# Kernel tuning notes

Hardware: AMD Instinct MI355X
Metric: run time of the kernel (lower is better)

The kernel has to match this reference:

```python
import jax, jax.numpy as jnp
import numpy as np


def setup_inputs() -> dict:
    key = jax.random.key(0)
    ks = jax.random.split(key, 7)
    B, I, H = 16384, 1024, 1024
    s = 1.0 / np.sqrt(H)
    return {
        "x": jax.random.normal(ks[0], (B, I), jnp.float32),
        "h_prev": jax.random.normal(ks[1], (B, H), jnp.float32),
        "c_prev": jax.random.normal(ks[2], (B, H), jnp.float32),
        "Wx": jax.random.normal(ks[3], (4, H, I), jnp.float32) * s,  # gates z,i,f,o
        "bx": jax.random.normal(ks[4], (4, H), jnp.float32) * s,
        "Rh": jax.random.normal(ks[5], (4, H, H), jnp.float32) * s,
        "bh": jax.random.normal(ks[6], (4, H), jnp.float32) * s,
    }


def reference(x, h_prev, c_prev, Wx, bx, Rh, bh):
    # Fused: 2 batched GEMMs for all 4 gates, then one elementwise block.
    # gates_x[g] = x @ Wx[g].T + bx[g]  (g in z,i,f,o), same for Rh/h_prev.
    gx = jnp.einsum('bi,ghi->gbh', x, Wx) + bx[:, None, :]       # [4,B,H]
    gh = jnp.einsum('bh,gkh->gbk', h_prev, Rh) + bh[:, None, :]  # [4,B,H]
    pre = gx + gh
    z = jnp.tanh(pre[0])
    i = jax.nn.sigmoid(pre[1])
    f = jax.nn.sigmoid(pre[2])
    o = jax.nn.sigmoid(pre[3])
    c = f * c_prev + i * z
    h = o * jnp.tanh(c)
    return (h, c)
```

## Files before the change

### kernel.cpp

```cpp
#include <hip/hip_runtime.h>
#include <stdint.h>

typedef __bf16 bf16;
typedef __bf16 bf16x8 __attribute__((ext_vector_type(8)));
typedef float  f32x4  __attribute__((ext_vector_type(4)));
typedef float  fvec4  __attribute__((ext_vector_type(4)));

#define B_DIM 16384
#define H_DIM 1024
#define K_DIM 2048

__device__ __forceinline__ void g2l16(const void* g, void* l) {
    __builtin_amdgcn_global_load_lds(
        (const __attribute__((address_space(1))) void*)g,
        (__attribute__((address_space(3))) void*)l,
        16, 0, 0);
}

__device__ __forceinline__ float sigm_fast(float x) {
    x = fminf(fmaxf(x, -40.f), 40.f);
    float e = __builtin_amdgcn_exp2f(-1.4426950408889634f * x);
    return __builtin_amdgcn_rcpf(1.0f + e);
}
__device__ __forceinline__ float tanh_fast(float x) {
    x = fminf(fmaxf(x, -40.f), 40.f);
    float e = __builtin_amdgcn_exp2f(-2.8853900817779268f * x);
    return (1.0f - e) * __builtin_amdgcn_rcpf(1.0f + e);
}

__device__ __forceinline__ bf16x8 cvt8(const float* __restrict__ src) {
    fvec4 a = __builtin_nontemporal_load((const fvec4*)src);
    fvec4 b = __builtin_nontemporal_load((const fvec4*)(src + 4));
    bf16x8 o = { (bf16)a.x, (bf16)a.y, (bf16)a.z, (bf16)a.w,
                 (bf16)b.x, (bf16)b.y, (bf16)b.z, (bf16)b.w };
    return o;
}

__global__ __launch_bounds__(256) void cvt_all(const float* __restrict__ x,
                                               const float* __restrict__ h,
                                               const float* __restrict__ Wx,
                                               const float* __restrict__ Rh,
                                               const float* __restrict__ bx,
                                               const float* __restrict__ bh,
                                               bf16* __restrict__ U,
                                               bf16* __restrict__ W,
                                               float* __restrict__ bb) {
    int b = blockIdx.x;
    if (b < 16384) {
        const float* src0 = (b < 8192) ? x : h;
        int half = (b < 8192) ? 0 : 1024;
        int gid  = (b & 8191) * 256 + threadIdx.x;
        int row  = gid >> 7;
        int c    = gid & 127;
        bf16x8 o = cvt8(src0 + ((size_t)row << 10) + (c << 3));
        *(bf16x8*)(U + ((size_t)row << 11) + half + (c << 3)) = o;
    } else {
        int gid = (b - 16384) * 256 + threadIdx.x;
        if (gid < 524288) {
            int row = gid >> 7;
            int c   = gid & 127;
            bf16x8 o = cvt8(Wx + ((size_t)row << 10) + (c << 3));
            *(bf16x8*)(W + ((size_t)row << 11) + (c << 3)) = o;
        } else {
            int g2  = gid - 524288;
            int row = g2 >> 7;
            int c   = g2 & 127;
            bf16x8 o = cvt8(Rh + ((size_t)row << 10) + (c << 3));
            *(bf16x8*)(W + ((size_t)row << 11) + 1024 + (c << 3)) = o;
        }
        if (gid < 4096) bb[gid] = bx[gid] + bh[gid];
    }
}

__global__ __launch_bounds__(256, 2)
void lstm_fused(const bf16* __restrict__ U, const bf16* __restrict__ W,
                const float* __restrict__ bb, const float* __restrict__ cprev,
                float* __restrict__ out) {
    __shared__ __align__(16) bf16 As[128 * 64];
    __shared__ __align__(16) bf16 Bs[128 * 64];

    const int tid  = threadIdx.x;
    const int wave = tid >> 6;
    const int lane = tid & 63;
    const int quad = lane >> 4;
    const int lc   = lane & 15;
    const int wm   = wave >> 1;
    const int wn   = wave & 1;

    int bid   = blockIdx.x;
    int xcd   = bid & 7;
    int j     = bid >> 3;
    int h_idx = xcd + ((j >> 7) << 3);
    int m_idx = j & 127;
    const int m0 = m_idx << 7;
    const int h0 = h_idx << 5;

    float bias[4];
#pragma unroll
    for (int g = 0; g < 4; ++g)
        bias[g] = bb[(g << 10) + h0 + (wn << 4) + lc];

    f32x4 acc[4][4];
#pragma unroll
    for (int mi = 0; mi < 4; ++mi)
#pragma unroll
        for (int ni = 0; ni < 4; ++ni)
            acc[mi][ni] = (f32x4){0.f, 0.f, 0.f, 0.f};

    const char* Ub = (const char*)U;
    const char* Wb = (const char*)W;

    for (int kb = 0; kb < K_DIM / 64; ++kb) {
        __syncthreads();
#pragma unroll
        for (int s = 0; s < 4; ++s) {
            int slot  = (s << 8) + (wave << 6) + lane;
            int row   = slot >> 3;
            int chunk = slot & 7;
            int colb  = (chunk ^ (row & 7)) << 4;
            int lb    = slot << 4;
            const char* ga = Ub + ((size_t)(m0 + row) << 12) + (kb << 7) + colb;
            g2l16(ga, (char*)As + lb);
            int gate = (row >> 4) & 3;
            int hh   = ((row >> 6) << 4) + (row & 15);
            int wrow = (gate << 10) + h0 + hh;
            const char* gb = Wb + ((size_t)wrow << 12) + (kb << 7) + colb;
            g2l16(gb, (char*)Bs + lb);
        }
        __syncthreads();

#pragma unroll
        for (int ks = 0; ks < 2; ++ks) {
            bf16x8 af[4];
            bf16x8 bfr[4];
#pragma unroll
            for (int mi = 0; mi < 4; ++mi) {
                int row = (wm << 6) + (mi << 4) + lc;
                int cs  = ((ks << 2) + quad) ^ (lc & 7);
                af[mi]  = *(const bf16x8*)(As + (row << 6) + (cs << 3));
            }
#pragma unroll
            for (int ni = 0; ni < 4; ++ni) {
                int row = (wn << 6) + (ni << 4) + lc;
                int cs  = ((ks << 2) + quad) ^ (lc & 7);
                bfr[ni] = *(const bf16x8*)(Bs + (row << 6) + (cs << 3));
            }
#pragma unroll
            for (int mi = 0; mi < 4; ++mi)
#pragma unroll
                for (int ni = 0; ni < 4; ++ni)
                    acc[mi][ni] = __builtin_amdgcn_mfma_f32_16x16x32_bf16(
                        af[mi], bfr[ni], acc[mi][ni], 0, 0, 0);
        }
    }

    float* out_h = out;
    float* out_c = out + (size_t)B_DIM * H_DIM;
    const int h = h0 + (wn << 4) + lc;
#pragma unroll
    for (int mi = 0; mi < 4; ++mi) {
#pragma unroll
        for (int r = 0; r < 4; ++r) {
            int brow  = m0 + (wm << 6) + (mi << 4) + (quad << 2) + r;
            size_t rb = (size_t)brow << 10;
            float zp = acc[mi][0][r] + bias[0];
            float ip = acc[mi][1][r] + bias[1];
            float fp = acc[mi][2][r] + bias[2];
            float op = acc[mi][3][r] + bias[3];
            float zz = tanh_fast(zp);
            float ii = sigm_fast(ip);
            float ff = sigm_fast(fp);
            float oo = sigm_fast(op);
            float cp = cprev[rb + h];
            float cn = ff * cp + ii * zz;
            float hn = oo * tanh_fast(cn);
            out_h[rb + h] = hn;
            out_c[rb + h] = cn;
        }
    }
}

extern "C" void kernel_launch(void* const* d_in, const int* in_sizes, int n_in,
                              void* d_out, int out_size, void* d_ws, size_t ws_size,
                              hipStream_t stream) {
    const float* x  = (const float*)d_in[0];
    const float* hp = (const float*)d_in[1];
    const float* cp = (const float*)d_in[2];
    const float* Wx = (const float*)d_in[3];
    const float* bx = (const float*)d_in[4];
    const float* Rh = (const float*)d_in[5];
    const float* bh = (const float*)d_in[6];

    bf16*  U  = (bf16*)d_ws;
    bf16*  W  = (bf16*)((char*)d_ws + (size_t)67108864);
    float* bb = (float*)((char*)d_ws + (size_t)67108864 + 16777216);

    cvt_all<<<20480, 256, 0, stream>>>(x, hp, Wx, Rh, bx, bh, U, W, bb);
    lstm_fused<<<4096, 256, 0, stream>>>(U, W, bb, cp, (float*)d_out);
}
```

Measured before the change: 580.5 us.

## Enlarge GEMM tile to 256x256 with double-buffered LDS and interleaved prefetch

Restructures the fused LSTM GEMM into 512-thread blocks computing 256x256 output tiles. Operand tiles are double-buffered in LDS, and loads for later k-steps are split into halves and interleaved with four MFMA quadrants per iteration. Barriers, explicit waitcnt and s_setprio are used to overlap global-to-LDS traffic with matrix math. The larger tile cuts the global load volume per FLOP. In exchange it uses 128KB of LDS and twice the accumulators, which limits occupancy, and the hand-written waitcnt counts add a correctness risk.

```diff
diff --git a/kernel.cpp b/kernel.cpp
--- a/kernel.cpp
+++ b/kernel.cpp
@@ -9,6 +9,7 @@
 #define B_DIM 16384
 #define H_DIM 1024
 #define K_DIM 2048
+#define NKT   32
 
 __device__ __forceinline__ void g2l16(const void* g, void* l) {
     __builtin_amdgcn_global_load_lds(
@@ -72,96 +73,180 @@
     }
 }
 
-__global__ __launch_bounds__(256, 2)
+__global__ __launch_bounds__(512, 2)
 void lstm_fused(const bf16* __restrict__ U, const bf16* __restrict__ W,
                 const float* __restrict__ bb, const float* __restrict__ cprev,
                 float* __restrict__ out) {
-    __shared__ __align__(16) bf16 As[128 * 64];
-    __shared__ __align__(16) bf16 Bs[128 * 64];
+    __shared__ __align__(16) bf16 As[2][256 * 64];
+    __shared__ __align__(16) bf16 Bs[2][256 * 64];
 
     const int tid  = threadIdx.x;
     const int wave = tid >> 6;
     const int lane = tid & 63;
     const int quad = lane >> 4;
     const int lc   = lane & 15;
-    const int wm   = wave >> 1;
-    const int wn   = wave & 1;
+    const int wm   = wave >> 2;
+    const int wn   = wave & 3;
 
     int bid   = blockIdx.x;
     int xcd   = bid & 7;
-    int j     = bid >> 3;
-    int h_idx = xcd + ((j >> 7) << 3);
-    int m_idx = j & 127;
-    const int m0 = m_idx << 7;
-    const int h0 = h_idx << 5;
-
-    float bias[4];
-#pragma unroll
-    for (int g = 0; g < 4; ++g)
-        bias[g] = bb[(g << 10) + h0 + (wn << 4) + lc];
-
-    f32x4 acc[4][4];
-#pragma unroll
-    for (int mi = 0; mi < 4; ++mi)
+    int t     = bid >> 3;
+    int h_idx = (xcd << 1) + (t >> 6);
+    int m_idx = t & 63;
+    const int m0 = m_idx << 8;
+    const int h0 = h_idx << 6;
+
+    uint32_t offA[2][2], offB[2][2];
+    uint32_t lofs[2];
+#pragma unroll
+    for (int ld = 0; ld < 2; ++ld) {
+        int slot  = (ld << 9) + tid;
+        int row   = slot >> 3;
+        int chunk = slot & 7;
+        int colb  = (chunk ^ (row & 7)) << 4;
+        lofs[ld]  = slot << 4;
+#pragma unroll
+        for (int hf = 0; hf < 2; ++hf) {
+            int arow = m0 + (hf << 7) + row;
+            offA[ld][hf] = ((uint32_t)arow << 12) + colb;
+            int br   = (hf << 7) + row;
+            int gate = (br >> 4) & 3;
+            int hl   = ((br >> 6) << 4) + (br & 15);
+            int wrow = (gate << 10) + h0 + hl;
+            offB[ld][hf] = ((uint32_t)wrow << 12) + colb;
+        }
+    }
+    const char* Ub = (const char*)U;
+    const char* Wb = (const char*)W;
+    char* AsB = (char*)As;
+    char* BsB = (char*)Bs;
+
+#define STG_A(hf, dbuf, ktt) do {                                              \
+        g2l16(Ub + offA[0][hf] + ((ktt) << 7),                                 \
+              AsB + ((dbuf) << 15) + ((hf) << 14) + lofs[0]);                  \
+        g2l16(Ub + offA[1][hf] + ((ktt) << 7),                                 \
+              AsB + ((dbuf) << 15) + ((hf) << 14) + lofs[1]);                  \
+    } while (0)
+#define STG_B(hf, dbuf, ktt) do {                                              \
+        g2l16(Wb + offB[0][hf] + ((ktt) << 7),                                 \
+              BsB + ((dbuf) << 15) + ((hf) << 14) + lofs[0]);                  \
+        g2l16(Wb + offB[1][hf] + ((ktt) << 7),                                 \
+              BsB + ((dbuf) << 15) + ((hf) << 14) + lofs[1]);                  \
+    } while (0)
+
+#define LDFRAG(BASEB, dbuf, row, ks)                                           \
+    (*(const bf16x8*)((BASEB) + ((dbuf) << 15) + ((row) << 7) +                \
+                      ((((((ks) << 2)) + quad) ^ (lc & 7)) << 4)))
+
+#define MFMA_Q(MIBASE, NIBASE)                                                 \
+    do {                                                                       \
+        _Pragma("unroll")                                                      \
+        for (int mi = 0; mi < 4; ++mi)                                         \
+            _Pragma("unroll")                                                  \
+            for (int ni = 0; ni < 2; ++ni)                                     \
+                _Pragma("unroll")                                              \
+                for (int ks = 0; ks < 2; ++ks)                                 \
+                    acc[(MIBASE) + mi][(NIBASE) + ni] =                        \
+                        __builtin_amdgcn_mfma_f32_16x16x32_bf16(               \
+                            a_[mi][ks], b_[(NIBASE) + ni][ks],                 \
+                            acc[(MIBASE) + mi][(NIBASE) + ni], 0, 0, 0);       \
+    } while (0)
+
+    f32x4 acc[8][4];
+#pragma unroll
+    for (int mi = 0; mi < 8; ++mi)
 #pragma unroll
         for (int ni = 0; ni < 4; ++ni)
             acc[mi][ni] = (f32x4){0.f, 0.f, 0.f, 0.f};
 
-    const char* Ub = (const char*)U;
-    const char* Wb = (const char*)W;
-
-    for (int kb = 0; kb < K_DIM / 64; ++kb) {
-        __syncthreads();
-#pragma unroll
-        for (int s = 0; s < 4; ++s) {
-            int slot  = (s << 8) + (wave << 6) + lane;
-            int row   = slot >> 3;
-            int chunk = slot & 7;
-            int colb  = (chunk ^ (row & 7)) << 4;
-            int lb    = slot << 4;
-            const char* ga = Ub + ((size_t)(m0 + row) << 12) + (kb << 7) + colb;
-            g2l16(ga, (char*)As + lb);
-            int gate = (row >> 4) & 3;
-            int hh   = ((row >> 6) << 4) + (row & 15);
-            int wrow = (gate << 10) + h0 + hh;
-            const char* gb = Wb + ((size_t)wrow << 12) + (kb << 7) + colb;
-            g2l16(gb, (char*)Bs + lb);
-        }
-        __syncthreads();
-
-#pragma unroll
-        for (int ks = 0; ks < 2; ++ks) {
-            bf16x8 af[4];
-            bf16x8 bfr[4];
-#pragma unroll
-            for (int mi = 0; mi < 4; ++mi) {
-                int row = (wm << 6) + (mi << 4) + lc;
-                int cs  = ((ks << 2) + quad) ^ (lc & 7);
-                af[mi]  = *(const bf16x8*)(As + (row << 6) + (cs << 3));
-            }
-#pragma unroll
-            for (int ni = 0; ni < 4; ++ni) {
-                int row = (wn << 6) + (ni << 4) + lc;
-                int cs  = ((ks << 2) + quad) ^ (lc & 7);
-                bfr[ni] = *(const bf16x8*)(Bs + (row << 6) + (cs << 3));
-            }
-#pragma unroll
-            for (int mi = 0; mi < 4; ++mi)
-#pragma unroll
-                for (int ni = 0; ni < 4; ++ni)
-                    acc[mi][ni] = __builtin_amdgcn_mfma_f32_16x16x32_bf16(
-                        af[mi], bfr[ni], acc[mi][ni], 0, 0, 0);
-        }
-    }
+    STG_B(0, 0, 0);
+    STG_A(0, 0, 0);
+    STG_A(1, 0, 0);
+    STG_B(1, 0, 0);
+    STG_B(0, 1, 1);
+    STG_A(0, 1, 1);
+    asm volatile("s_waitcnt vmcnt(4)" ::: "memory");
+    __builtin_amdgcn_s_barrier();
+
+    const int rA0 = (wm << 7) + lc;
+    const int rB0 = (wn << 6) + lc;
+
+    bf16x8 a_[4][2];
+    bf16x8 b_[4][2];
+
+#pragma clang loop unroll(disable)
+    for (int kt = 0; kt < NKT; ++kt) {
+        const int buf = kt & 1;
+
+#pragma unroll
+        for (int mi = 0; mi < 4; ++mi) {
+            a_[mi][0] = LDFRAG(AsB, buf, rA0 + (mi << 4), 0);
+            a_[mi][1] = LDFRAG(AsB, buf, rA0 + (mi << 4), 1);
+        }
+#pragma unroll
+        for (int ni = 0; ni < 2; ++ni) {
+            b_[ni][0] = LDFRAG(BsB, buf, rB0 + (ni << 4), 0);
+            b_[ni][1] = LDFRAG(BsB, buf, rB0 + (ni << 4), 1);
+        }
+        if (kt < NKT - 1) STG_A(1, buf ^ 1, kt + 1);
+        __builtin_amdgcn_s_barrier();
+        asm volatile("s_waitcnt lgkmcnt(0)" ::: "memory");
+        __builtin_amdgcn_s_setprio(1);
+        MFMA_Q(0, 0);
+        __builtin_amdgcn_s_setprio(0);
+        __builtin_amdgcn_s_barrier();
+
+#pragma unroll
+        for (int ni = 2; ni < 4; ++ni) {
+            b_[ni][0] = LDFRAG(BsB, buf, rB0 + (ni << 4), 0);
+            b_[ni][1] = LDFRAG(BsB, buf, rB0 + (ni << 4), 1);
+        }
+        if (kt < NKT - 1) STG_B(1, buf ^ 1, kt + 1);
+        __builtin_amdgcn_s_barrier();
+        asm volatile("s_waitcnt lgkmcnt(0)" ::: "memory");
+        __builtin_amdgcn_s_setprio(1);
+        MFMA_Q(0, 2);
+        __builtin_amdgcn_s_setprio(0);
+        __builtin_amdgcn_s_barrier();
+
+#pragma unroll
+        for (int mi = 0; mi < 4; ++mi) {
+            a_[mi][0] = LDFRAG(AsB, buf, rA0 + 64 + (mi << 4), 0);
+            a_[mi][1] = LDFRAG(AsB, buf, rA0 + 64 + (mi << 4), 1);
+        }
+        if (kt < NKT - 2) STG_B(0, buf, kt + 2);
+        __builtin_amdgcn_s_barrier();
+        asm volatile("s_waitcnt lgkmcnt(0)" ::: "memory");
+        __builtin_amdgcn_s_setprio(1);
+        MFMA_Q(4, 0);
+        __builtin_amdgcn_s_setprio(0);
+        __builtin_amdgcn_s_barrier();
+
+        if (kt < NKT - 2) STG_A(0, buf, kt + 2);
+        __builtin_amdgcn_s_barrier();
+        __builtin_amdgcn_s_setprio(1);
+        MFMA_Q(4, 2);
+        __builtin_amdgcn_s_setprio(0);
+        if (kt < NKT - 2) {
+            asm volatile("s_waitcnt vmcnt(4)" ::: "memory");
+        } else if (kt == NKT - 2) {
+            asm volatile("s_waitcnt vmcnt(0)" ::: "memory");
+        }
+        __builtin_amdgcn_s_barrier();
+    }
+
+    const int h = h0 + (wn << 4) + lc;
+    float bias[4];
+#pragma unroll
+    for (int g = 0; g < 4; ++g) bias[g] = bb[(g << 10) + h];
 
     float* out_h = out;
     float* out_c = out + (size_t)B_DIM * H_DIM;
-    const int h = h0 + (wn << 4) + lc;
-#pragma unroll
-    for (int mi = 0; mi < 4; ++mi) {
+#pragma unroll
+    for (int mi = 0; mi < 8; ++mi) {
 #pragma unroll
         for (int r = 0; r < 4; ++r) {
-            int brow  = m0 + (wm << 6) + (mi << 4) + (quad << 2) + r;
+            int brow  = m0 + (wm << 7) + (mi << 4) + (quad << 2) + r;
             size_t rb = (size_t)brow << 10;
             float zp = acc[mi][0][r] + bias[0];
             float ip = acc[mi][1][r] + bias[1];
@@ -196,5 +281,5 @@
     float* bb = (float*)((char*)d_ws + (size_t)67108864 + 16777216);
 
     cvt_all<<<20480, 256, 0, stream>>>(x, hp, Wx, Rh, bx, bh, U, W, bb);
-    lstm_fused<<<4096, 256, 0, stream>>>(U, W, bb, cp, (float*)d_out);
-}
+    lstm_fused<<<1024, 512, 0, stream>>>(U, W, bb, cp, (float*)d_out);
+}
```

Result: faster. 535.3 us (-7.8%).
